# Kernel tuning notes

Hardware: AMD Instinct MI355X
Metric: run time of the kernel (lower is better)

The kernel has to match this reference:

```python
import jax, jax.numpy as jnp
import numpy as np

H = 16  # num_heads

def setup_inputs() -> dict:
    key = jax.random.key(0)
    ks = jax.random.split(key, 5)
    C = 1024
    x = jax.random.normal(ks[0], (4, 2048, C), dtype=jnp.float32)
    # torch nn.Linear params: weight (out, in), bias (out,)
    qkv_w = jax.random.normal(ks[1], (3 * C, C), dtype=jnp.float32) * (C ** -0.5)
    qkv_b = jnp.zeros((3 * C,), dtype=jnp.float32)
    proj_w = jax.random.normal(ks[2], (C, C), dtype=jnp.float32) * (C ** -0.5)
    proj_b = jnp.zeros((C,), dtype=jnp.float32)
    return {"x": x, "qkv_w": qkv_w, "qkv_b": qkv_b, "proj_w": proj_w, "proj_b": proj_b}

def reference(x, qkv_w, qkv_b, proj_w, proj_b):
    B, T, C = x.shape
    hd = C // H
    scale = hd ** -0.5
    qkv = x @ qkv_w.T + qkv_b                      # [B,T,3C]
    qkv = qkv.reshape(B, T, 3, H, hd)
    q, k, v = jnp.moveaxis(qkv, 2, 0)              # each [B,T,H,hd]
    q = q.transpose(0, 2, 1, 3)                    # [B,H,T,hd]
    k = k.transpose(0, 2, 1, 3)
    v = v.transpose(0, 2, 1, 3)
    attn = jnp.einsum('bhqd,bhkd->bhqk', q, k) * scale
    attn = jax.nn.softmax(attn, axis=-1)           # dropout is identity at eval
    out = jnp.einsum('bhqk,bhkd->bhqd', attn, v)   # [B,H,T,hd]
    out = out.transpose(0, 2, 1, 3).reshape(B, T, C)
    return out @ proj_w.T + proj_b
```

## Files before the change

### kernel.cpp

```cpp
#include <hip/hip_runtime.h>


typedef _Float16 f16x8 __attribute__((ext_vector_type(8)));
typedef _Float16 f16x4 __attribute__((ext_vector_type(4)));
typedef float f32x4 __attribute__((ext_vector_type(4)));

__device__ __forceinline__ uint4 cvt8h(const float* p) {
    float4 a = *(const float4*)p, b = *(const float4*)(p + 4);
    union { _Float16 h[8]; uint4 u; } t;
    t.h[0] = (_Float16)a.x; t.h[1] = (_Float16)a.y;
    t.h[2] = (_Float16)a.z; t.h[3] = (_Float16)a.w;
    t.h[4] = (_Float16)b.x; t.h[5] = (_Float16)b.y;
    t.h[6] = (_Float16)b.z; t.h[7] = (_Float16)b.w;
    return t.u;
}

template <int CTRL>
__device__ __forceinline__ float dppmov(float x) {
    return __int_as_float(
        __builtin_amdgcn_update_dpp(0, __float_as_int(x), CTRL, 0xF, 0xF, true));
}
__device__ __forceinline__ float rsum16(float x) {
    x += dppmov<0x128>(x);
    x += dppmov<0x124>(x);
    x += dppmov<0x122>(x);
    x += dppmov<0x121>(x);
    return x;
}

#define LSTR 40

__global__ __launch_bounds__(256) void cvt_fp16(
    const float* __restrict__ x, const float* __restrict__ w1,
    const float* __restrict__ w2,
    _Float16* __restrict__ xh, _Float16* __restrict__ w1h,
    _Float16* __restrict__ w2h)
{
    const int g = blockIdx.x * 256 + threadIdx.x;
    const float* src; _Float16* dst; int off;
    if (g < 1048576)      { src = x;  dst = xh;  off = g; }
    else if (g < 1441792) { src = w1; dst = w1h; off = g - 1048576; }
    else                  { src = w2; dst = w2h; off = g - 1441792; }
    const size_t e = (size_t)off * 8;
    *(uint4*)(dst + e) = cvt8h(src + e);
}

__global__ __launch_bounds__(256) void qkv_gemm(
    const _Float16* __restrict__ X, const _Float16* __restrict__ W,
    const float* __restrict__ Bias,
    _Float16* __restrict__ qws, _Float16* __restrict__ kws,
    _Float16* __restrict__ vtws)
{
    __shared__ _Float16 sA[128 * LSTR];
    __shared__ _Float16 sB[128 * LSTR];
    const int tid = threadIdx.x;
    const int wave = tid >> 6, lane = tid & 63;
    const int wm = (wave >> 1) * 64, wn = (wave & 1) * 64;
    const int lr = lane & 15, lq = lane >> 4;
    const int m0 = blockIdx.y * 128, n0 = blockIdx.x * 128;
    const int srow = tid >> 2, scol = (tid & 3) * 8;
    const int s = n0 >> 10;

    f32x4 acc[4][4] = {};

    const _Float16* gA0 = X + (size_t)(m0 + srow) * 1024 + scol;
    const _Float16* gA1 = gA0 + (size_t)64 * 1024;
    const _Float16* gB0 = W + (size_t)(n0 + srow) * 1024 + scol;
    const _Float16* gB1 = gB0 + (size_t)64 * 1024;

    for (int k0 = 0; k0 < 1024; k0 += 32) {
        uint4 a0 = *(const uint4*)(gA0 + k0);
        uint4 a1 = *(const uint4*)(gA1 + k0);
        uint4 b0 = *(const uint4*)(gB0 + k0);
        uint4 b1 = *(const uint4*)(gB1 + k0);
        __syncthreads();
        *(uint4*)&sA[srow * LSTR + scol] = a0;
        *(uint4*)&sA[(srow + 64) * LSTR + scol] = a1;
        *(uint4*)&sB[srow * LSTR + scol] = b0;
        *(uint4*)&sB[(srow + 64) * LSTR + scol] = b1;
        __syncthreads();
        f16x8 af[4], bf[4];
        #pragma unroll
        for (int i = 0; i < 4; ++i) {
            af[i] = *(const f16x8*)&sA[(wm + i * 16 + lr) * LSTR + lq * 8];
            bf[i] = *(const f16x8*)&sB[(wn + i * 16 + lr) * LSTR + lq * 8];
        }
        #pragma unroll
        for (int mi = 0; mi < 4; ++mi)
            #pragma unroll
            for (int ni = 0; ni < 4; ++ni)
                acc[mi][ni] = __builtin_amdgcn_mfma_f32_16x16x32_f16(
                    af[mi], bf[ni], acc[mi][ni], 0, 0, 0);
    }

    #pragma unroll
    for (int mi = 0; mi < 4; ++mi) {
        #pragma unroll
        for (int ni = 0; ni < 4; ++ni) {
            const int n = n0 + wn + ni * 16 + lr;
            const float bv = Bias[n];
            const int h = (n >> 6) & 15, d = n & 63;
            const int mbase = m0 + wm + mi * 16 + lq * 4;
            const int b = mbase >> 11, t0 = mbase & 2047;
            const int bh = b * 16 + h;
            if (s == 0) {
                #pragma unroll
                for (int r = 0; r < 4; ++r)
                    qws[((size_t)bh * 2048 + t0 + r) * 64 + d] =
                        (_Float16)((acc[mi][ni][r] + bv) * 0.18033688f);
            } else if (s == 1) {
                #pragma unroll
                for (int r = 0; r < 4; ++r)
                    kws[((size_t)bh * 2048 + t0 + r) * 64 + d] =
                        (_Float16)(acc[mi][ni][r] + bv);
            } else {
                f16x4 pk;
                #pragma unroll
                for (int r = 0; r < 4; ++r) pk[r] = (_Float16)(acc[mi][ni][r] + bv);
                *(f16x4*)&vtws[((size_t)bh * 64 + d) * 2048 + t0] = pk;
            }
        }
    }
}

__global__ __launch_bounds__(256, 4) void attn_kernel(
    const _Float16* __restrict__ qws,
    const _Float16* __restrict__ kws,
    const _Float16* __restrict__ vtws,
    _Float16* __restrict__ ows)
{
    __shared__ _Float16 sP[4][32][72];
    __shared__ _Float16 sK[64][72];
    __shared__ _Float16 sV[64][72];
    const int bh = blockIdx.y, qb = blockIdx.x;
    const int tid = threadIdx.x, wave = tid >> 6, lane = tid & 63;
    const int lr = lane & 15, lq = lane >> 4;

    _Float16* sQ = &sP[0][0][0];
    {
        const _Float16* gq = qws + ((size_t)bh * 2048 + qb * 128) * 64;
        for (int i = tid; i < 1024; i += 256)
            *(uint4*)&sQ[i * 8] = *(const uint4*)&gq[i * 8];
    }
    __syncthreads();
    f16x8 aQ[2][2];
    #pragma unroll
    for (int mb = 0; mb < 2; ++mb)
        #pragma unroll
        for (int ks = 0; ks < 2; ++ks)
            aQ[mb][ks] = *(const f16x8*)&sQ[(wave * 32 + mb * 16 + lr) * 64 + ks * 32 + lq * 8];

    f32x4 o[2][4] = {};
    float l_loc[2][4] = {};

    for (int kt = 0; kt < 32; ++kt) {
        const _Float16* gk = kws + ((size_t)bh * 2048 + kt * 64) * 64;
        const _Float16* gv = vtws + (size_t)bh * 64 * 2048 + kt * 64;
        if (kt) __syncthreads();
        for (int i = tid; i < 512; i += 256) {
            const int row = i >> 3, c = (i & 7) * 8;
            *(uint4*)&sK[row][c] = *(const uint4*)&gk[row * 64 + c];
            *(uint4*)&sV[row][c] = *(const uint4*)&gv[(size_t)row * 2048 + c];
        }
        __syncthreads();

        f16x8 bK[2][4];
        #pragma unroll
        for (int ks = 0; ks < 2; ++ks)
            #pragma unroll
            for (int nb = 0; nb < 4; ++nb)
                bK[ks][nb] = *(const f16x8*)&sK[nb * 16 + lr][ks * 32 + lq * 8];
        f32x4 sc[2][4] = {};
        #pragma unroll
        for (int mb = 0; mb < 2; ++mb)
            #pragma unroll
            for (int nb = 0; nb < 4; ++nb) {
                sc[mb][nb] = __builtin_amdgcn_mfma_f32_16x16x32_f16(
                    aQ[mb][0], bK[0][nb], sc[mb][nb], 0, 0, 0);
                sc[mb][nb] = __builtin_amdgcn_mfma_f32_16x16x32_f16(
                    aQ[mb][1], bK[1][nb], sc[mb][nb], 0, 0, 0);
            }

        #pragma unroll
        for (int mb = 0; mb < 2; ++mb)
            #pragma unroll
            for (int nb = 0; nb < 4; ++nb)
                #pragma unroll
                for (int reg = 0; reg < 4; ++reg) {
                    const float p = exp2f(sc[mb][nb][reg]);
                    l_loc[mb][reg] += p;
                    sP[wave][mb * 16 + lq * 4 + reg][nb * 16 + lr] = (_Float16)p;
                }

        f16x8 vA[2][4], pB[2][2];
        #pragma unroll
        for (int ks = 0; ks < 2; ++ks)
            #pragma unroll
            for (int db = 0; db < 4; ++db)
                vA[ks][db] = *(const f16x8*)&sV[db * 16 + lr][ks * 32 + lq * 8];
        #pragma unroll
        for (int mb = 0; mb < 2; ++mb)
            #pragma unroll
            for (int ks = 0; ks < 2; ++ks)
                pB[mb][ks] = *(const f16x8*)&sP[wave][mb * 16 + lr][ks * 32 + lq * 8];
        #pragma unroll
        for (int mb = 0; mb < 2; ++mb)
            #pragma unroll
            for (int db = 0; db < 4; ++db) {
                o[mb][db] = __builtin_amdgcn_mfma_f32_16x16x32_f16(
                    vA[0][db], pB[mb][0], o[mb][db], 0, 0, 0);
                o[mb][db] = __builtin_amdgcn_mfma_f32_16x16x32_f16(
                    vA[1][db], pB[mb][1], o[mb][db], 0, 0, 0);
            }
    }

    __syncthreads();
    float* sL = (float*)&sK[0][0];
    #pragma unroll
    for (int mb = 0; mb < 2; ++mb)
        #pragma unroll
        for (int reg = 0; reg < 4; ++reg) {
            const float t = rsum16(l_loc[mb][reg]);
            if (lr == 0) sL[wave * 32 + mb * 16 + lq * 4 + reg] = t;
        }
    const int b = bh >> 4, h = bh & 15;
    #pragma unroll
    for (int mb = 0; mb < 2; ++mb) {
        const float linv = 1.0f / sL[wave * 32 + mb * 16 + lr];
        const int t = qb * 128 + wave * 32 + mb * 16 + lr;
        #pragma unroll
        for (int db = 0; db < 4; ++db) {
            f16x4 pk;
            #pragma unroll
            for (int reg = 0; reg < 4; ++reg)
                pk[reg] = (_Float16)(o[mb][db][reg] * linv);
            *(f16x4*)&ows[((size_t)(b * 2048 + t)) * 1024 + h * 64 + db * 16 + lq * 4] = pk;
        }
    }
}

__global__ __launch_bounds__(256) void proj_gemm(
    const _Float16* __restrict__ A, const _Float16* __restrict__ W,
    const float* __restrict__ Bias, float* __restrict__ out)
{
    __shared__ _Float16 sA[128 * LSTR];
    __shared__ _Float16 sB[128 * LSTR];
    const int tid = threadIdx.x;
    const int wave = tid >> 6, lane = tid & 63;
    const int wm = (wave >> 1) * 64, wn = (wave & 1) * 64;
    const int lr = lane & 15, lq = lane >> 4;
    const int m0 = blockIdx.y * 128, n0 = blockIdx.x * 128;
    const int srow = tid >> 2, scol = (tid & 3) * 8;

    f32x4 acc[4][4] = {};

    const _Float16* gA0 = A + (size_t)(m0 + srow) * 1024 + scol;
    const _Float16* gA1 = gA0 + (size_t)64 * 1024;
    const _Float16* gB0 = W + (size_t)(n0 + srow) * 1024 + scol;
    const _Float16* gB1 = gB0 + (size_t)64 * 1024;

    for (int k0 = 0; k0 < 1024; k0 += 32) {
        uint4 a0 = *(const uint4*)(gA0 + k0);
        uint4 a1 = *(const uint4*)(gA1 + k0);
        uint4 b0 = *(const uint4*)(gB0 + k0);
        uint4 b1 = *(const uint4*)(gB1 + k0);
        __syncthreads();
        *(uint4*)&sA[srow * LSTR + scol] = a0;
        *(uint4*)&sA[(srow + 64) * LSTR + scol] = a1;
        *(uint4*)&sB[srow * LSTR + scol] = b0;
        *(uint4*)&sB[(srow + 64) * LSTR + scol] = b1;
        __syncthreads();
        f16x8 af[4], bf[4];
        #pragma unroll
        for (int i = 0; i < 4; ++i) {
            af[i] = *(const f16x8*)&sA[(wm + i * 16 + lr) * LSTR + lq * 8];
            bf[i] = *(const f16x8*)&sB[(wn + i * 16 + lr) * LSTR + lq * 8];
        }
        #pragma unroll
        for (int mi = 0; mi < 4; ++mi)
            #pragma unroll
            for (int ni = 0; ni < 4; ++ni)
                acc[mi][ni] = __builtin_amdgcn_mfma_f32_16x16x32_f16(
                    af[mi], bf[ni], acc[mi][ni], 0, 0, 0);
    }

    #pragma unroll
    for (int mi = 0; mi < 4; ++mi) {
        #pragma unroll
        for (int ni = 0; ni < 4; ++ni) {
            const int n = n0 + wn + ni * 16 + lr;
            const float bv = Bias[n];
            #pragma unroll
            for (int r = 0; r < 4; ++r) {
                const int m = m0 + wm + mi * 16 + lq * 4 + r;
                out[(size_t)m * 1024 + n] = acc[mi][ni][r] + bv;
            }
        }
    }
}

extern "C" void kernel_launch(void* const* d_in, const int* in_sizes, int n_in,
                              void* d_out, int out_size, void* d_ws, size_t ws_size,
                              hipStream_t stream) {
    const float* x      = (const float*)d_in[0];
    const float* qkv_w  = (const float*)d_in[1];
    const float* qkv_b  = (const float*)d_in[2];
    const float* proj_w = (const float*)d_in[3];
    const float* proj_b = (const float*)d_in[4];
    float* out = (float*)d_out;

    char* ws = (char*)d_ws;
    _Float16* qws  = (_Float16*)(ws);
    _Float16* kws  = (_Float16*)(ws + 16777216u);
    _Float16* vtws = (_Float16*)(ws + 33554432u);
    _Float16* ows  = (_Float16*)(ws + 50331648u);
    _Float16* Xh   = (_Float16*)(ws + 67108864u);
    _Float16* Wqh  = (_Float16*)(ws + 83886080u);
    _Float16* Wph  = (_Float16*)(ws + 90177536u);

    cvt_fp16<<<dim3(6144), 256, 0, stream>>>(x, qkv_w, proj_w, Xh, Wqh, Wph);
    qkv_gemm<<<dim3(24, 64), 256, 0, stream>>>(Xh, Wqh, qkv_b, qws, kws, vtws);
    attn_kernel<<<dim3(16, 64), 256, 0, stream>>>(qws, kws, vtws, ows);
    proj_gemm<<<dim3(8, 64), 256, 0, stream>>>(ows, Wph, proj_b, out);
}
```

Baseline: 328.2 us.

## Use direct global-to-LDS loads in GEMMs and prefetch K/V tiles in attention

```diff
diff --git a/kernel.cpp b/kernel.cpp
--- a/kernel.cpp
+++ b/kernel.cpp
@@ -28,7 +28,11 @@
     return x;
 }
 
-#define LSTR 40
+__device__ __forceinline__ void dma16(const _Float16* g, _Float16* l) {
+    __builtin_amdgcn_global_load_lds(
+        (const __attribute__((address_space(1))) unsigned int*)g,
+        (__attribute__((address_space(3))) unsigned int*)l, 16, 0, 0);
+}
 
 __global__ __launch_bounds__(256) void cvt_fp16(
     const float* __restrict__ x, const float* __restrict__ w1,
@@ -51,39 +55,35 @@
     _Float16* __restrict__ qws, _Float16* __restrict__ kws,
     _Float16* __restrict__ vtws)
 {
-    __shared__ _Float16 sA[128 * LSTR];
-    __shared__ _Float16 sB[128 * LSTR];
+    __shared__ _Float16 sA[128 * 32];
+    __shared__ _Float16 sB[128 * 32];
     const int tid = threadIdx.x;
     const int wave = tid >> 6, lane = tid & 63;
     const int wm = (wave >> 1) * 64, wn = (wave & 1) * 64;
     const int lr = lane & 15, lq = lane >> 4;
     const int m0 = blockIdx.y * 128, n0 = blockIdx.x * 128;
-    const int srow = tid >> 2, scol = (tid & 3) * 8;
     const int s = n0 >> 10;
 
+    const int drow = wave * 16 + (lane >> 2);
+    const int dcol = (lane & 3) * 8;
+    _Float16* ldsA = sA + wave * 512;
+    _Float16* ldsB = sB + wave * 512;
+    const _Float16* gA = X + (size_t)(m0 + drow) * 1024 + dcol;
+    const _Float16* gB = W + (size_t)(n0 + drow) * 1024 + dcol;
+
     f32x4 acc[4][4] = {};
 
-    const _Float16* gA0 = X + (size_t)(m0 + srow) * 1024 + scol;
-    const _Float16* gA1 = gA0 + (size_t)64 * 1024;
-    const _Float16* gB0 = W + (size_t)(n0 + srow) * 1024 + scol;
-    const _Float16* gB1 = gB0 + (size_t)64 * 1024;
-
     for (int k0 = 0; k0 < 1024; k0 += 32) {
-        uint4 a0 = *(const uint4*)(gA0 + k0);
-        uint4 a1 = *(const uint4*)(gA1 + k0);
-        uint4 b0 = *(const uint4*)(gB0 + k0);
-        uint4 b1 = *(const uint4*)(gB1 + k0);
-        __syncthreads();
-        *(uint4*)&sA[srow * LSTR + scol] = a0;
-        *(uint4*)&sA[(srow + 64) * LSTR + scol] = a1;
-        *(uint4*)&sB[srow * LSTR + scol] = b0;
-        *(uint4*)&sB[(srow + 64) * LSTR + scol] = b1;
+        dma16(gA + k0, ldsA);
+        dma16(gA + (size_t)64 * 1024 + k0, ldsA + 2048);
+        dma16(gB + k0, ldsB);
+        dma16(gB + (size_t)64 * 1024 + k0, ldsB + 2048);
         __syncthreads();
         f16x8 af[4], bf[4];
         #pragma unroll
         for (int i = 0; i < 4; ++i) {
-            af[i] = *(const f16x8*)&sA[(wm + i * 16 + lr) * LSTR + lq * 8];
-            bf[i] = *(const f16x8*)&sB[(wn + i * 16 + lr) * LSTR + lq * 8];
+            af[i] = *(const f16x8*)&sA[(wm + i * 16 + lr) * 32 + lq * 8];
+            bf[i] = *(const f16x8*)&sB[(wn + i * 16 + lr) * 32 + lq * 8];
         }
         #pragma unroll
         for (int mi = 0; mi < 4; ++mi)
@@ -91,6 +91,7 @@
             for (int ni = 0; ni < 4; ++ni)
                 acc[mi][ni] = __builtin_amdgcn_mfma_f32_16x16x32_f16(
                     af[mi], bf[ni], acc[mi][ni], 0, 0, 0);
+        __syncthreads();
     }
 
     #pragma unroll
@@ -129,10 +130,12 @@
     const _Float16* __restrict__ vtws,
     _Float16* __restrict__ ows)
 {
-    __shared__ _Float16 sP[4][32][72];
+    __shared__ _Float16 sP[4][32][76];
     __shared__ _Float16 sK[64][72];
     __shared__ _Float16 sV[64][72];
-    const int bh = blockIdx.y, qb = blockIdx.x;
+    const int bid = blockIdx.x;
+    const int bh = (bid & 7) * 8 + ((bid >> 3) & 7);
+    const int qb = bid >> 6;
     const int tid = threadIdx.x, wave = tid >> 6, lane = tid & 63;
     const int lr = lane & 15, lq = lane >> 4;
 
@@ -150,19 +153,37 @@
         for (int ks = 0; ks < 2; ++ks)
             aQ[mb][ks] = *(const f16x8*)&sQ[(wave * 32 + mb * 16 + lr) * 64 + ks * 32 + lq * 8];
 
+    const int srow = tid >> 3, scc = (tid & 7) * 8;
+    const _Float16* gkb = kws + (size_t)bh * 2048 * 64;
+    const _Float16* gvb = vtws + (size_t)bh * 64 * 2048;
+    uint4 kr0, kr1, vr0, vr1;
+    {
+        const _Float16* gk = gkb;
+        const _Float16* gv = gvb;
+        kr0 = *(const uint4*)&gk[srow * 64 + scc];
+        kr1 = *(const uint4*)&gk[(srow + 32) * 64 + scc];
+        vr0 = *(const uint4*)&gv[(size_t)srow * 2048 + scc];
+        vr1 = *(const uint4*)&gv[(size_t)(srow + 32) * 2048 + scc];
+    }
+
     f32x4 o[2][4] = {};
     float l_loc[2][4] = {};
 
     for (int kt = 0; kt < 32; ++kt) {
-        const _Float16* gk = kws + ((size_t)bh * 2048 + kt * 64) * 64;
-        const _Float16* gv = vtws + (size_t)bh * 64 * 2048 + kt * 64;
-        if (kt) __syncthreads();
-        for (int i = tid; i < 512; i += 256) {
-            const int row = i >> 3, c = (i & 7) * 8;
-            *(uint4*)&sK[row][c] = *(const uint4*)&gk[row * 64 + c];
-            *(uint4*)&sV[row][c] = *(const uint4*)&gv[(size_t)row * 2048 + c];
-        }
-        __syncthreads();
+        __syncthreads();
+        *(uint4*)&sK[srow][scc] = kr0;
+        *(uint4*)&sK[srow + 32][scc] = kr1;
+        *(uint4*)&sV[srow][scc] = vr0;
+        *(uint4*)&sV[srow + 32][scc] = vr1;
+        __syncthreads();
+        if (kt < 31) {
+            const _Float16* gk = gkb + (kt + 1) * 64 * 64;
+            const _Float16* gv = gvb + (kt + 1) * 64;
+            kr0 = *(const uint4*)&gk[srow * 64 + scc];
+            kr1 = *(const uint4*)&gk[(srow + 32) * 64 + scc];
+            vr0 = *(const uint4*)&gv[(size_t)srow * 2048 + scc];
+            vr1 = *(const uint4*)&gv[(size_t)(srow + 32) * 2048 + scc];
+        }
 
         f16x8 bK[2][4];
         #pragma unroll
@@ -201,8 +222,12 @@
         #pragma unroll
         for (int mb = 0; mb < 2; ++mb)
             #pragma unroll
-            for (int ks = 0; ks < 2; ++ks)
-                pB[mb][ks] = *(const f16x8*)&sP[wave][mb * 16 + lr][ks * 32 + lq * 8];
+            for (int ks = 0; ks < 2; ++ks) {
+                const _Float16* p = &sP[wave][mb * 16 + lr][ks * 32 + lq * 8];
+                f16x4 lo = *(const f16x4*)p;
+                f16x4 hi = *(const f16x4*)(p + 4);
+                pB[mb][ks] = __builtin_shufflevector(lo, hi, 0, 1, 2, 3, 4, 5, 6, 7);
+            }
         #pragma unroll
         for (int mb = 0; mb < 2; ++mb)
             #pragma unroll
@@ -243,38 +268,34 @@
     const _Float16* __restrict__ A, const _Float16* __restrict__ W,
     const float* __restrict__ Bias, float* __restrict__ out)
 {
-    __shared__ _Float16 sA[128 * LSTR];
-    __shared__ _Float16 sB[128 * LSTR];
+    __shared__ _Float16 sA[128 * 32];
+    __shared__ _Float16 sB[128 * 32];
     const int tid = threadIdx.x;
     const int wave = tid >> 6, lane = tid & 63;
     const int wm = (wave >> 1) * 64, wn = (wave & 1) * 64;
     const int lr = lane & 15, lq = lane >> 4;
     const int m0 = blockIdx.y * 128, n0 = blockIdx.x * 128;
-    const int srow = tid >> 2, scol = (tid & 3) * 8;
+
+    const int drow = wave * 16 + (lane >> 2);
+    const int dcol = (lane & 3) * 8;
+    _Float16* ldsA = sA + wave * 512;
+    _Float16* ldsB = sB + wave * 512;
+    const _Float16* gA = A + (size_t)(m0 + drow) * 1024 + dcol;
+    const _Float16* gB = W + (size_t)(n0 + drow) * 1024 + dcol;
 
     f32x4 acc[4][4] = {};
 
-    const _Float16* gA0 = A + (size_t)(m0 + srow) * 1024 + scol;
-    const _Float16* gA1 = gA0 + (size_t)64 * 1024;
-    const _Float16* gB0 = W + (size_t)(n0 + srow) * 1024 + scol;
-    const _Float16* gB1 = gB0 + (size_t)64 * 1024;
-
     for (int k0 = 0; k0 < 1024; k0 += 32) {
-        uint4 a0 = *(const uint4*)(gA0 + k0);
-        uint4 a1 = *(const uint4*)(gA1 + k0);
-        uint4 b0 = *(const uint4*)(gB0 + k0);
-        uint4 b1 = *(const uint4*)(gB1 + k0);
-        __syncthreads();
-        *(uint4*)&sA[srow * LSTR + scol] = a0;
-        *(uint4*)&sA[(srow + 64) * LSTR + scol] = a1;
-        *(uint4*)&sB[srow * LSTR + scol] = b0;
-        *(uint4*)&sB[(srow + 64) * LSTR + scol] = b1;
+        dma16(gA + k0, ldsA);
+        dma16(gA + (size_t)64 * 1024 + k0, ldsA + 2048);
+        dma16(gB + k0, ldsB);
+        dma16(gB + (size_t)64 * 1024 + k0, ldsB + 2048);
         __syncthreads();
         f16x8 af[4], bf[4];
         #pragma unroll
         for (int i = 0; i < 4; ++i) {
-            af[i] = *(const f16x8*)&sA[(wm + i * 16 + lr) * LSTR + lq * 8];
-            bf[i] = *(const f16x8*)&sB[(wn + i * 16 + lr) * LSTR + lq * 8];
+            af[i] = *(const f16x8*)&sA[(wm + i * 16 + lr) * 32 + lq * 8];
+            bf[i] = *(const f16x8*)&sB[(wn + i * 16 + lr) * 32 + lq * 8];
         }
         #pragma unroll
         for (int mi = 0; mi < 4; ++mi)
@@ -282,6 +303,7 @@
             for (int ni = 0; ni < 4; ++ni)
                 acc[mi][ni] = __builtin_amdgcn_mfma_f32_16x16x32_f16(
                     af[mi], bf[ni], acc[mi][ni], 0, 0, 0);
+        __syncthreads();
     }
 
     #pragma unroll
@@ -320,6 +342,6 @@
 
     cvt_fp16<<<dim3(6144), 256, 0, stream>>>(x, qkv_w, proj_w, Xh, Wqh, Wph);
     qkv_gemm<<<dim3(24, 64), 256, 0, stream>>>(Xh, Wqh, qkv_b, qws, kws, vtws);
-    attn_kernel<<<dim3(16, 64), 256, 0, stream>>>(qws, kws, vtws, ows);
+    attn_kernel<<<dim3(1024), 256, 0, stream>>>(qws, kws, vtws, ows);
     proj_gemm<<<dim3(8, 64), 256, 0, stream>>>(ows, Wph, proj_b, out);
 }
```

After: 362.7 us. 10.5% more time.
